# Performance work log

Measured on AMD Instinct MI355X. Metric: run time of the kernel, lower is better.

## Reference

```python
import jax, jax.numpy as jnp
import numpy as np

PLAYERS = 8
DMODEL = 256          # cfg.dmodel (per-embedding dim)
DK = 1024             # cfg.dk
WINDOW = 4096         # cfg.window == T here
A_SPACE = 64
DFULL = DMODEL * 2 * PLAYERS   # 4096, the concatenated model dim


def _positional_encoding(T, dmodel):
    # i = 1/10000^(2j/dmodel); pe[:, ::2]=sin(pos*i), pe[:, 1::2]=cos(pos*i)
    i = 1.0 / jnp.power(jnp.float32(10000.0), jnp.arange(0, dmodel, 2, dtype=jnp.float32) / dmodel)
    pos = jnp.arange(T, dtype=jnp.float32)[:, None]
    pe = jnp.zeros((T, dmodel), dtype=jnp.float32)
    pe = pe.at[:, ::2].set(jnp.sin(pos * i))
    pe = pe.at[:, 1::2].set(jnp.cos(pos * i))
    return pe


def setup_inputs() -> dict:
    key = jax.random.key(0)
    ks = jax.random.split(key, 12)
    n_rows = WINDOW * 2 * PLAYERS  # 65536 one-hot rows
    idx = jax.random.randint(ks[0], (n_rows,), 0, PLAYERS + 1)
    obs = jax.nn.one_hot(idx, PLAYERS + 1, dtype=jnp.int32)
    std = 2.0 / (5.0 * DFULL)  # torch.normal(0, var) uses var as std in the source
    return {
        "obs": obs,
        "o_emb": jax.random.normal(ks[1], (PLAYERS + 1, DMODEL), jnp.float32),
        "d_emb": jax.random.normal(ks[2], (PLAYERS + 1, DMODEL), jnp.float32),
        "WQ": jax.random.normal(ks[3], (DFULL, DK), jnp.float32) * std,
        "WK": jax.random.normal(ks[4], (DFULL, DK), jnp.float32) * std,
        "WV": jax.random.normal(ks[5], (DFULL, DK), jnp.float32) * std,
        "WO": jax.random.normal(ks[6], (DK, DK), jnp.float32) * std,
        "Wo_pol": jax.random.normal(ks[7], (A_SPACE, DK), jnp.float32) * 0.02,
        "bo_pol": jnp.zeros((A_SPACE,), jnp.float32),
        "Wd_pol": jax.random.normal(ks[8], (A_SPACE, DK), jnp.float32) * 0.02,
        "bd_pol": jnp.zeros((A_SPACE,), jnp.float32),
        "Wv": jax.random.normal(ks[9], (1, DK), jnp.float32) * 0.02,
        "bv": jnp.zeros((1,), jnp.float32),
    }


def reference(obs, o_emb, d_emb, WQ, WK, WV, WO, Wo_pol, bo_pol, Wd_pol, bd_pol, Wv, bv):
    obs2 = obs.reshape(-1, PLAYERS + 1)
    # torch.where(row == 1)[1] on one-hot rows == argmax
    idx_o = jnp.argmax(obs2[::2], axis=1)   # [T*players]
    idx_d = jnp.argmax(obs2[1::2], axis=1)  # [T*players]
    emb = jnp.concatenate([o_emb[idx_o], d_emb[idx_d]], axis=1)  # [T*players, 2*dmodel]
    x = emb.reshape(-1, DFULL) * jnp.sqrt(jnp.float32(DMODEL))    # [T, DFULL]
    T = x.shape[0]
    x = x + _positional_encoding(T, DFULL)
    q = x @ WQ  # [T, DK]
    k = x @ WK
    v = x @ WV
    att = jax.nn.softmax((q @ k.T) / jnp.sqrt(jnp.float32(DK)), axis=-1)  # [T, T]
    o = (att @ v) @ WO  # [T, DK]
    h = jax.nn.relu(o[-1])  # last position only, [DK]
    o_logits = h @ Wo_pol.T + bo_pol  # [A_SPACE]
    d_logits = h @ Wd_pol.T + bd_pol  # [A_SPACE]
    value = h @ Wv.T + bv             # [1]
    return (o_logits, d_logits, value)
```

## Files before the change

kernel.cpp:

```cpp
#include <hip/hip_runtime.h>
#include <stdint.h>

#define T_WIN   4096
#define DFULL   4096
#define DK      1024

static const size_t IDX_OFF  = 0;
static const size_t XL_OFF   = 65536;
static const size_t FRQ_OFF  = 81920;
static const size_t KQ_OFF   = 90112;
static const size_t S_OFF    = 106496;
static const size_t ATT_OFF  = 122880;
static const size_t QP_OFF   = 139264;
static const size_t AXPE_OFF = 155648;
static const size_t W_OFF    = 172032;
static const size_t CTX_OFF  = 173056;
static const size_t OL_OFF   = 177152;

#define LOG2_10000 13.287712379549449f

__global__ void idx_k(const int* __restrict__ obs,
                      const float* __restrict__ o_emb,
                      const float* __restrict__ d_emb,
                      unsigned char* __restrict__ idxb,
                      float* __restrict__ xlast,
                      float* __restrict__ freqt,
                      float* __restrict__ zbase) {
    int b = blockIdx.x, tid = threadIdx.x;
    if (b < 256) {
        int g = b * 256 + tid;
        const int* r = obs + (size_t)g * 9;
        int id = 0;
        #pragma unroll
        for (int j = 1; j < 9; ++j) id += j * r[j];
        int t = g >> 4;
        int p = (g >> 1) & 7, which = g & 1;
        idxb[t * 16 + which * 8 + p] = (unsigned char)id;
    } else if (b == 256) {
        __shared__ int lidx[16];
        if (tid < 16) {
            int row = 65520 + tid;
            const int* r = obs + (size_t)row * 9;
            int id = 0;
            #pragma unroll
            for (int j = 1; j < 9; ++j) id += j * r[j];
            int p = tid >> 1, which = tid & 1;
            lidx[which * 8 + p] = id;
        }
        __syncthreads();
        #pragma unroll
        for (int i = 0; i < 16; ++i) {
            int c = tid + 256 * i;
            int p = c >> 9, rr = c & 511;
            int seg, r; const float* tab;
            if (rr < 256) { seg = p;     r = rr;       tab = o_emb; }
            else          { seg = 8 + p; r = rr - 256; tab = d_emb; }
            float e = tab[lidx[seg] * 256 + r];
            float f = exp2f(-((float)(c & ~1) * (1.0f / 4096.0f)) * LOG2_10000);
            float sv, cv;
            __sincosf(4095.0f * f, &sv, &cv);
            xlast[c] = e * 16.0f + ((c & 1) ? cv : sv);
        }
    } else {
        float4 z4 = {0.f, 0.f, 0.f, 0.f};
        float4* z = (float4*)zbase;
        for (int i = tid; i < 2624; i += 256) z[i] = z4;
        for (int i = tid; i < 2048; i += 256)
            freqt[i] = exp2f(-((float)(2 * i) * (1.0f / 4096.0f)) * LOG2_10000);
    }
}

__global__ void q_k(const float* __restrict__ xlast,
                    const float* __restrict__ WQ,
                    float* __restrict__ qp) {
    int kc = blockIdx.x, tid = threadIdx.x;
    const float4* W4 = (const float4*)WQ;
    float4 acc = {0.f, 0.f, 0.f, 0.f};
    int kb = kc * 16;
    #pragma unroll
    for (int k = 0; k < 16; ++k) {
        float xv = xlast[kb + k];
        float4 w = W4[(size_t)(kb + k) * 256 + tid];
        acc.x += xv * w.x; acc.y += xv * w.y;
        acc.z += xv * w.z; acc.w += xv * w.w;
    }
    float* dst = qp + (kc >> 6) * 1024 + tid * 4;
    atomicAdd(dst + 0, acc.x);
    atomicAdd(dst + 1, acc.y);
    atomicAdd(dst + 2, acc.z);
    atomicAdd(dst + 3, acc.w);
}

__global__ void kq_k(const float* __restrict__ WK,
                     const float* __restrict__ qp,
                     float* __restrict__ kq) {
    __shared__ float4 qls[256];
    int tid = threadIdx.x;
    const float4* p4 = (const float4*)qp;
    float4 a = p4[tid], b = p4[256 + tid], c = p4[512 + tid], d = p4[768 + tid];
    qls[tid] = {a.x + b.x + c.x + d.x, a.y + b.y + c.y + d.y,
                a.z + b.z + c.z + d.z, a.w + b.w + c.w + d.w};
    __syncthreads();
    int wave = tid >> 6, lane = tid & 63;
    int cc = blockIdx.x * 4 + wave;
    const float4* W4 = (const float4*)(WK + (size_t)cc * DK);
    float acc = 0.0f;
    #pragma unroll
    for (int i = 0; i < 4; ++i) {
        float4 w = W4[i * 64 + lane];
        float4 q = qls[i * 64 + lane];
        acc += w.x * q.x + w.y * q.y + w.z * q.z + w.w * q.w;
    }
    #pragma unroll
    for (int off = 32; off; off >>= 1) acc += __shfl_down(acc, off, 64);
    if (lane == 0) kq[cc] = acc * (1.0f / 32.0f);
}

__global__ __launch_bounds__(256) void scores_k(
        const float* __restrict__ kq,
        const float* __restrict__ o_emb, const float* __restrict__ d_emb,
        const float* __restrict__ freqt,
        const unsigned char* __restrict__ idxb,
        float* __restrict__ s) {
    __shared__ float lkq[4096];
    __shared__ float lemb[18 * 257];
    __shared__ float lfrq[2048];
    __shared__ float ldot[144];
    __shared__ float lped[256];
    int tid = threadIdx.x, blk = blockIdx.x;
    for (int i = tid; i < 1024; i += 256)
        ((float4*)lkq)[i] = ((const float4*)kq)[i];
    for (int i = tid; i < 512; i += 256)
        ((float4*)lfrq)[i] = ((const float4*)freqt)[i];
    for (int i = tid; i < 4608; i += 256) {
        int row = i >> 8, r = i & 255;
        lemb[row * 257 + r] = (row < 9) ? o_emb[row * 256 + r]
                                        : d_emb[(row - 9) * 256 + r];
    }
    __syncthreads();
    if (tid < 144) {
        int seg = tid / 9, id = tid % 9;
        int base = (seg < 8) ? seg * 512 : (seg - 8) * 512 + 256;
        const float* e = lemb + ((seg < 8) ? id : (9 + id)) * 257;
        float a = 0.0f;
        for (int rr = 0; rr < 256; ++rr) {
            int r = (rr + seg * 4) & 255;
            a += e[r] * lkq[base + r];
        }
        ldot[tid] = 16.0f * a;
    }
    int tt = tid >> 4, sub = tid & 15;
    int t = blk * 16 + tt;
    float acc = 0.0f;
    for (int jj = 0; jj < 128; ++jj) {
        int j = sub * 128 + ((jj + 2 * sub) & 127);
        float f = lfrq[j];
        float sv, cv;
        __sincosf((float)t * f, &sv, &cv);
        acc += sv * lkq[2 * j] + cv * lkq[2 * j + 1];
    }
    lped[tt * 16 + sub] = acc;
    __syncthreads();
    if (tid < 16) {
        int t2 = blk * 16 + tid;
        float tot = 0.0f;
        #pragma unroll
        for (int i = 0; i < 16; ++i) tot += lped[tid * 16 + i];
        const uint32_t* ip = (const uint32_t*)(idxb + t2 * 16);
        uint32_t u0 = ip[0], u1 = ip[1], u2 = ip[2], u3 = ip[3];
        #pragma unroll
        for (int seg = 0; seg < 16; ++seg) {
            uint32_t u = (seg < 4) ? u0 : (seg < 8) ? u1 : (seg < 12) ? u2 : u3;
            int id = (u >> ((seg & 3) * 8)) & 0xFF;
            tot += ldot[seg * 9 + id];
        }
        s[t2] = tot;
    }
}

__global__ void softmax_k(const float* __restrict__ s, float* __restrict__ att) {
    __shared__ float redm[16], reds[16];
    int tid = threadIdx.x;
    float v0 = s[tid], v1 = s[tid + 1024], v2 = s[tid + 2048], v3 = s[tid + 3072];
    float m = fmaxf(fmaxf(v0, v1), fmaxf(v2, v3));
    #pragma unroll
    for (int off = 32; off; off >>= 1) m = fmaxf(m, __shfl_down(m, off, 64));
    if ((tid & 63) == 0) redm[tid >> 6] = m;
    __syncthreads();
    if (tid == 0) {
        float mm = redm[0];
        for (int i = 1; i < 16; ++i) mm = fmaxf(mm, redm[i]);
        redm[0] = mm;
    }
    __syncthreads();
    m = redm[0];
    float e0 = expf(v0 - m), e1 = expf(v1 - m), e2 = expf(v2 - m), e3 = expf(v3 - m);
    float sum = e0 + e1 + e2 + e3;
    #pragma unroll
    for (int off = 32; off; off >>= 1) sum += __shfl_down(sum, off, 64);
    if ((tid & 63) == 0) reds[tid >> 6] = sum;
    __syncthreads();
    if (tid == 0) {
        float ss = 0.0f;
        for (int i = 0; i < 16; ++i) ss += reds[i];
        reds[0] = ss;
    }
    __syncthreads();
    float inv = 1.0f / reds[0];
    att[tid] = e0 * inv; att[tid + 1024] = e1 * inv;
    att[tid + 2048] = e2 * inv; att[tid + 3072] = e3 * inv;
}

__global__ void att_post_k(const float* __restrict__ att,
                           const float* __restrict__ freqt,
                           const unsigned char* __restrict__ idxb,
                           float* __restrict__ weight,
                           float* __restrict__ axpe) {
    __shared__ float lh[144];
    int tid = threadIdx.x, b = blockIdx.x;
    if (tid < 144) lh[tid] = 0.0f;
    __syncthreads();
    #pragma unroll
    for (int i = 0; i < 2; ++i) {
        int it = tid + 256 * i;
        int t = b * 32 + (it >> 4), seg = it & 15;
        int id = idxb[t * 16 + seg];
        atomicAdd(&lh[seg * 9 + id], att[t]);
    }
    __syncthreads();
    if (tid < 144) atomicAdd(&weight[tid], lh[tid]);
    int g = b * 256 + tid;
    int j = g & 2047;
    int t0 = (g >> 11) * 256;
    float f = freqt[j];
    float sf, cf;
    __sincosf(f, &sf, &cf);
    float ss = 0.0f, sc = 0.0f;
    float sv = 0.f, cv = 0.f;
    for (int i = 0; i < 256; ++i) {
        if ((i & 63) == 0) __sincosf((float)(t0 + i) * f, &sv, &cv);
        float a = att[t0 + i];
        ss += a * sv; sc += a * cv;
        float ns = sv * cf + cv * sf;
        cv = cv * cf - sv * sf;
        sv = ns;
    }
    atomicAdd(&axpe[2 * j], ss);
    atomicAdd(&axpe[2 * j + 1], sc);
}

__global__ void ctxv_k(const float* __restrict__ weight,
                       const float* __restrict__ axpe,
                       const float* __restrict__ o_emb,
                       const float* __restrict__ d_emb,
                       const float* __restrict__ WV,
                       float* __restrict__ ctx) {
    __shared__ float lax[128];
    int tid = threadIdx.x;
    int cc = blockIdx.x >> 2, nc = blockIdx.x & 3;
    if (tid < 128) {
        int c = cc * 128 + tid;
        int p = c >> 9, rr = c & 511;
        int seg, r; const float* tab;
        if (rr < 256) { seg = p;     r = rr;       tab = o_emb; }
        else          { seg = 8 + p; r = rr - 256; tab = d_emb; }
        float a = 0.0f;
        #pragma unroll
        for (int id = 0; id < 9; ++id)
            a += weight[seg * 9 + id] * tab[id * 256 + r];
        lax[tid] = axpe[c] + 16.0f * a;
    }
    __syncthreads();
    int n = nc * 256 + tid;
    const float* Wp = WV + (size_t)cc * 128 * DK + n;
    float acc = 0.0f;
    for (int i = 0; i < 128; ++i)
        acc += lax[i] * Wp[(size_t)i * DK];
    atomicAdd(&ctx[n], acc);
}

__global__ void olast_k(const float* __restrict__ ctx,
                        const float* __restrict__ WO,
                        float* __restrict__ ol) {
    __shared__ float lc[64];
    int tid = threadIdx.x;
    int jc = blockIdx.x >> 2, mc = blockIdx.x & 3;
    if (tid < 64) lc[tid] = ctx[jc * 64 + tid];
    __syncthreads();
    int m = mc * 256 + tid;
    const float* Wp = WO + (size_t)jc * 64 * DK + m;
    float acc = 0.0f;
    for (int j = 0; j < 64; ++j)
        acc += lc[j] * Wp[(size_t)j * DK];
    atomicAdd(&ol[m], acc);
}

__global__ void heads_k(const float* __restrict__ ol,
                        const float* __restrict__ Wo_pol, const float* __restrict__ bo_pol,
                        const float* __restrict__ Wd_pol, const float* __restrict__ bd_pol,
                        const float* __restrict__ Wv,     const float* __restrict__ bv,
                        float* __restrict__ out) {
    __shared__ float red[4];
    int o = blockIdx.x;
    const float* W; float b;
    if (o < 64)       { W = Wo_pol + (size_t)o * DK;        b = bo_pol[o]; }
    else if (o < 128) { W = Wd_pol + (size_t)(o - 64) * DK; b = bd_pol[o - 64]; }
    else              { W = Wv;                              b = bv[0]; }
    float s = 0.0f;
    for (int m = threadIdx.x; m < DK; m += 256)
        s += fmaxf(ol[m], 0.0f) * W[m];
    #pragma unroll
    for (int off = 32; off; off >>= 1) s += __shfl_down(s, off, 64);
    int wave = threadIdx.x >> 6, lane = threadIdx.x & 63;
    if (lane == 0) red[wave] = s;
    __syncthreads();
    if (threadIdx.x == 0) out[o] = red[0] + red[1] + red[2] + red[3] + b;
}

extern "C" void kernel_launch(void* const* d_in, const int* in_sizes, int n_in,
                              void* d_out, int out_size, void* d_ws, size_t ws_size,
                              hipStream_t stream) {
    const int*   obs    = (const int*)  d_in[0];
    const float* o_emb  = (const float*)d_in[1];
    const float* d_emb  = (const float*)d_in[2];
    const float* WQ     = (const float*)d_in[3];
    const float* WK     = (const float*)d_in[4];
    const float* WV     = (const float*)d_in[5];
    const float* WO     = (const float*)d_in[6];
    const float* Wo_pol = (const float*)d_in[7];
    const float* bo_pol = (const float*)d_in[8];
    const float* Wd_pol = (const float*)d_in[9];
    const float* bd_pol = (const float*)d_in[10];
    const float* Wv     = (const float*)d_in[11];
    const float* bv     = (const float*)d_in[12];
    float* out = (float*)d_out;

    char* ws = (char*)d_ws;
    unsigned char* idxb = (unsigned char*)(ws + IDX_OFF);
    float* xlast = (float*)(ws + XL_OFF);
    float* freqt = (float*)(ws + FRQ_OFF);
    float* kq    = (float*)(ws + KQ_OFF);
    float* s     = (float*)(ws + S_OFF);
    float* att   = (float*)(ws + ATT_OFF);
    float* qp    = (float*)(ws + QP_OFF);
    float* axpe  = (float*)(ws + AXPE_OFF);
    float* wgt   = (float*)(ws + W_OFF);
    float* ctx   = (float*)(ws + CTX_OFF);
    float* ol    = (float*)(ws + OL_OFF);

    idx_k<<<258, 256, 0, stream>>>(obs, o_emb, d_emb, idxb, xlast, freqt, qp);
    q_k<<<256, 256, 0, stream>>>(xlast, WQ, qp);
    kq_k<<<1024, 256, 0, stream>>>(WK, qp, kq);
    scores_k<<<256, 256, 0, stream>>>(kq, o_emb, d_emb, freqt, idxb, s);
    softmax_k<<<1, 1024, 0, stream>>>(s, att);
    att_post_k<<<128, 256, 0, stream>>>(att, freqt, idxb, wgt, axpe);
    ctxv_k<<<128, 256, 0, stream>>>(wgt, axpe, o_emb, d_emb, WV, ctx);
    olast_k<<<64, 256, 0, stream>>>(ctx, WO, ol);
    heads_k<<<129, 256, 0, stream>>>(ol, Wo_pol, bo_pol, Wd_pol, bd_pol, Wv, bv, out);
}
```

Before: 164.1 us.

## Fuse all stages into one cooperative persistent kernel with grid syncs

Replaces nine separate kernel launches with a single cooperative kernel of 256 blocks that runs the stages in sequence, separated by grid-wide barriers. The point is to remove per-launch overhead and the gaps between small kernels. The single-block softmax is now computed redundantly in every block so attention weights no longer go through global memory. The xlast buffer is dropped in favour of shared memory in the Q stage. The costs are grid-sync latency and idle blocks in the later, smaller stages.

```diff
diff --git a/kernel.cpp b/kernel.cpp
--- a/kernel.cpp
+++ b/kernel.cpp
@@ -1,360 +1,328 @@
 #include <hip/hip_runtime.h>
+#include <hip/hip_cooperative_groups.h>
 #include <stdint.h>
+
+namespace cg = cooperative_groups;
 
 #define T_WIN   4096
 #define DFULL   4096
 #define DK      1024
+#define GRID    256
+#define LOG2_10000 13.287712379549449f
 
 static const size_t IDX_OFF  = 0;
-static const size_t XL_OFF   = 65536;
-static const size_t FRQ_OFF  = 81920;
-static const size_t KQ_OFF   = 90112;
-static const size_t S_OFF    = 106496;
-static const size_t ATT_OFF  = 122880;
-static const size_t QP_OFF   = 139264;
-static const size_t AXPE_OFF = 155648;
-static const size_t W_OFF    = 172032;
-static const size_t CTX_OFF  = 173056;
-static const size_t OL_OFF   = 177152;
-
-#define LOG2_10000 13.287712379549449f
-
-__global__ void idx_k(const int* __restrict__ obs,
-                      const float* __restrict__ o_emb,
-                      const float* __restrict__ d_emb,
-                      unsigned char* __restrict__ idxb,
-                      float* __restrict__ xlast,
-                      float* __restrict__ freqt,
-                      float* __restrict__ zbase) {
+static const size_t FRQ_OFF  = 65536;
+static const size_t KQ_OFF   = 73728;
+static const size_t S_OFF    = 90112;
+static const size_t QP_OFF   = 106496;
+static const size_t AXPE_OFF = 122880;
+static const size_t W_OFF    = 139264;
+static const size_t CTX_OFF  = 140288;
+static const size_t OL_OFF   = 144384;
+
+struct Par {
+    const int* obs;
+    const float* o_emb; const float* d_emb;
+    const float* WQ; const float* WK; const float* WV; const float* WO;
+    const float* Wo_pol; const float* bo_pol;
+    const float* Wd_pol; const float* bd_pol;
+    const float* Wv; const float* bv;
+    unsigned char* idxb;
+    float* freqt; float* kq; float* s;
+    float* qp; float* axpe; float* weight; float* ctx; float* ol;
+    float* out;
+};
+
+__global__ void __launch_bounds__(256) mega_k(Par p) {
+    cg::grid_group grid = cg::this_grid();
+    __shared__ __align__(16) float smem[11264];
     int b = blockIdx.x, tid = threadIdx.x;
-    if (b < 256) {
+    int wave = tid >> 6, lane = tid & 63;
+
+    {
         int g = b * 256 + tid;
-        const int* r = obs + (size_t)g * 9;
+        const int* r = p.obs + (size_t)g * 9;
         int id = 0;
         #pragma unroll
         for (int j = 1; j < 9; ++j) id += j * r[j];
-        int t = g >> 4;
-        int p = (g >> 1) & 7, which = g & 1;
-        idxb[t * 16 + which * 8 + p] = (unsigned char)id;
-    } else if (b == 256) {
-        __shared__ int lidx[16];
+        int t = g >> 4, pl = (g >> 1) & 7, which = g & 1;
+        p.idxb[t * 16 + which * 8 + pl] = (unsigned char)id;
+        if (b == 1)
+            for (int i = tid; i < 10496; i += 256) p.qp[i] = 0.0f;
+        if (b == 2)
+            for (int i = tid; i < 2048; i += 256)
+                p.freqt[i] = exp2f(-((float)(2 * i) * (1.0f / 4096.0f)) * LOG2_10000);
+    }
+    grid.sync();
+
+    {
+        int kb = b * 16;
+        int pl = kb >> 9, rr = kb & 511;
+        const float* tab; int r0, which;
+        if (rr < 256) { tab = p.o_emb; r0 = rr;       which = 0; }
+        else          { tab = p.d_emb; r0 = rr - 256; which = 1; }
         if (tid < 16) {
-            int row = 65520 + tid;
-            const int* r = obs + (size_t)row * 9;
+            int row = 65520 + pl * 2 + which;
+            const int* r = p.obs + (size_t)row * 9;
             int id = 0;
             #pragma unroll
             for (int j = 1; j < 9; ++j) id += j * r[j];
-            int p = tid >> 1, which = tid & 1;
-            lidx[which * 8 + p] = id;
-        }
-        __syncthreads();
-        #pragma unroll
-        for (int i = 0; i < 16; ++i) {
-            int c = tid + 256 * i;
-            int p = c >> 9, rr = c & 511;
-            int seg, r; const float* tab;
-            if (rr < 256) { seg = p;     r = rr;       tab = o_emb; }
-            else          { seg = 8 + p; r = rr - 256; tab = d_emb; }
-            float e = tab[lidx[seg] * 256 + r];
+            int c = kb + tid;
             float f = exp2f(-((float)(c & ~1) * (1.0f / 4096.0f)) * LOG2_10000);
             float sv, cv;
             __sincosf(4095.0f * f, &sv, &cv);
-            xlast[c] = e * 16.0f + ((c & 1) ? cv : sv);
-        }
-    } else {
-        float4 z4 = {0.f, 0.f, 0.f, 0.f};
-        float4* z = (float4*)zbase;
-        for (int i = tid; i < 2624; i += 256) z[i] = z4;
-        for (int i = tid; i < 2048; i += 256)
-            freqt[i] = exp2f(-((float)(2 * i) * (1.0f / 4096.0f)) * LOG2_10000);
-    }
-}
-
-__global__ void q_k(const float* __restrict__ xlast,
-                    const float* __restrict__ WQ,
-                    float* __restrict__ qp) {
-    int kc = blockIdx.x, tid = threadIdx.x;
-    const float4* W4 = (const float4*)WQ;
-    float4 acc = {0.f, 0.f, 0.f, 0.f};
-    int kb = kc * 16;
-    #pragma unroll
-    for (int k = 0; k < 16; ++k) {
-        float xv = xlast[kb + k];
-        float4 w = W4[(size_t)(kb + k) * 256 + tid];
-        acc.x += xv * w.x; acc.y += xv * w.y;
-        acc.z += xv * w.z; acc.w += xv * w.w;
-    }
-    float* dst = qp + (kc >> 6) * 1024 + tid * 4;
-    atomicAdd(dst + 0, acc.x);
-    atomicAdd(dst + 1, acc.y);
-    atomicAdd(dst + 2, acc.z);
-    atomicAdd(dst + 3, acc.w);
-}
-
-__global__ void kq_k(const float* __restrict__ WK,
-                     const float* __restrict__ qp,
-                     float* __restrict__ kq) {
-    __shared__ float4 qls[256];
-    int tid = threadIdx.x;
-    const float4* p4 = (const float4*)qp;
-    float4 a = p4[tid], b = p4[256 + tid], c = p4[512 + tid], d = p4[768 + tid];
-    qls[tid] = {a.x + b.x + c.x + d.x, a.y + b.y + c.y + d.y,
-                a.z + b.z + c.z + d.z, a.w + b.w + c.w + d.w};
-    __syncthreads();
-    int wave = tid >> 6, lane = tid & 63;
-    int cc = blockIdx.x * 4 + wave;
-    const float4* W4 = (const float4*)(WK + (size_t)cc * DK);
-    float acc = 0.0f;
-    #pragma unroll
-    for (int i = 0; i < 4; ++i) {
-        float4 w = W4[i * 64 + lane];
-        float4 q = qls[i * 64 + lane];
-        acc += w.x * q.x + w.y * q.y + w.z * q.z + w.w * q.w;
-    }
-    #pragma unroll
-    for (int off = 32; off; off >>= 1) acc += __shfl_down(acc, off, 64);
-    if (lane == 0) kq[cc] = acc * (1.0f / 32.0f);
-}
-
-__global__ __launch_bounds__(256) void scores_k(
-        const float* __restrict__ kq,
-        const float* __restrict__ o_emb, const float* __restrict__ d_emb,
-        const float* __restrict__ freqt,
-        const unsigned char* __restrict__ idxb,
-        float* __restrict__ s) {
-    __shared__ float lkq[4096];
-    __shared__ float lemb[18 * 257];
-    __shared__ float lfrq[2048];
-    __shared__ float ldot[144];
-    __shared__ float lped[256];
-    int tid = threadIdx.x, blk = blockIdx.x;
-    for (int i = tid; i < 1024; i += 256)
-        ((float4*)lkq)[i] = ((const float4*)kq)[i];
-    for (int i = tid; i < 512; i += 256)
-        ((float4*)lfrq)[i] = ((const float4*)freqt)[i];
-    for (int i = tid; i < 4608; i += 256) {
-        int row = i >> 8, r = i & 255;
-        lemb[row * 257 + r] = (row < 9) ? o_emb[row * 256 + r]
-                                        : d_emb[(row - 9) * 256 + r];
-    }
-    __syncthreads();
-    if (tid < 144) {
-        int seg = tid / 9, id = tid % 9;
-        int base = (seg < 8) ? seg * 512 : (seg - 8) * 512 + 256;
-        const float* e = lemb + ((seg < 8) ? id : (9 + id)) * 257;
-        float a = 0.0f;
-        for (int rr = 0; rr < 256; ++rr) {
-            int r = (rr + seg * 4) & 255;
-            a += e[r] * lkq[base + r];
-        }
-        ldot[tid] = 16.0f * a;
-    }
-    int tt = tid >> 4, sub = tid & 15;
-    int t = blk * 16 + tt;
-    float acc = 0.0f;
-    for (int jj = 0; jj < 128; ++jj) {
-        int j = sub * 128 + ((jj + 2 * sub) & 127);
-        float f = lfrq[j];
-        float sv, cv;
-        __sincosf((float)t * f, &sv, &cv);
-        acc += sv * lkq[2 * j] + cv * lkq[2 * j + 1];
-    }
-    lped[tt * 16 + sub] = acc;
-    __syncthreads();
-    if (tid < 16) {
-        int t2 = blk * 16 + tid;
-        float tot = 0.0f;
-        #pragma unroll
-        for (int i = 0; i < 16; ++i) tot += lped[tid * 16 + i];
-        const uint32_t* ip = (const uint32_t*)(idxb + t2 * 16);
-        uint32_t u0 = ip[0], u1 = ip[1], u2 = ip[2], u3 = ip[3];
-        #pragma unroll
-        for (int seg = 0; seg < 16; ++seg) {
-            uint32_t u = (seg < 4) ? u0 : (seg < 8) ? u1 : (seg < 12) ? u2 : u3;
-            int id = (u >> ((seg & 3) * 8)) & 0xFF;
-            tot += ldot[seg * 9 + id];
-        }
-        s[t2] = tot;
-    }
-}
-
-__global__ void softmax_k(const float* __restrict__ s, float* __restrict__ att) {
-    __shared__ float redm[16], reds[16];
-    int tid = threadIdx.x;
-    float v0 = s[tid], v1 = s[tid + 1024], v2 = s[tid + 2048], v3 = s[tid + 3072];
-    float m = fmaxf(fmaxf(v0, v1), fmaxf(v2, v3));
-    #pragma unroll
-    for (int off = 32; off; off >>= 1) m = fmaxf(m, __shfl_down(m, off, 64));
-    if ((tid & 63) == 0) redm[tid >> 6] = m;
-    __syncthreads();
-    if (tid == 0) {
-        float mm = redm[0];
-        for (int i = 1; i < 16; ++i) mm = fmaxf(mm, redm[i]);
-        redm[0] = mm;
-    }
-    __syncthreads();
-    m = redm[0];
-    float e0 = expf(v0 - m), e1 = expf(v1 - m), e2 = expf(v2 - m), e3 = expf(v3 - m);
-    float sum = e0 + e1 + e2 + e3;
-    #pragma unroll
-    for (int off = 32; off; off >>= 1) sum += __shfl_down(sum, off, 64);
-    if ((tid & 63) == 0) reds[tid >> 6] = sum;
-    __syncthreads();
-    if (tid == 0) {
-        float ss = 0.0f;
-        for (int i = 0; i < 16; ++i) ss += reds[i];
-        reds[0] = ss;
-    }
-    __syncthreads();
-    float inv = 1.0f / reds[0];
-    att[tid] = e0 * inv; att[tid + 1024] = e1 * inv;
-    att[tid + 2048] = e2 * inv; att[tid + 3072] = e3 * inv;
-}
-
-__global__ void att_post_k(const float* __restrict__ att,
-                           const float* __restrict__ freqt,
-                           const unsigned char* __restrict__ idxb,
-                           float* __restrict__ weight,
-                           float* __restrict__ axpe) {
-    __shared__ float lh[144];
-    int tid = threadIdx.x, b = blockIdx.x;
-    if (tid < 144) lh[tid] = 0.0f;
-    __syncthreads();
-    #pragma unroll
-    for (int i = 0; i < 2; ++i) {
-        int it = tid + 256 * i;
-        int t = b * 32 + (it >> 4), seg = it & 15;
-        int id = idxb[t * 16 + seg];
-        atomicAdd(&lh[seg * 9 + id], att[t]);
-    }
-    __syncthreads();
-    if (tid < 144) atomicAdd(&weight[tid], lh[tid]);
-    int g = b * 256 + tid;
-    int j = g & 2047;
-    int t0 = (g >> 11) * 256;
-    float f = freqt[j];
-    float sf, cf;
-    __sincosf(f, &sf, &cf);
-    float ss = 0.0f, sc = 0.0f;
-    float sv = 0.f, cv = 0.f;
-    for (int i = 0; i < 256; ++i) {
-        if ((i & 63) == 0) __sincosf((float)(t0 + i) * f, &sv, &cv);
-        float a = att[t0 + i];
-        ss += a * sv; sc += a * cv;
-        float ns = sv * cf + cv * sf;
-        cv = cv * cf - sv * sf;
-        sv = ns;
-    }
-    atomicAdd(&axpe[2 * j], ss);
-    atomicAdd(&axpe[2 * j + 1], sc);
-}
-
-__global__ void ctxv_k(const float* __restrict__ weight,
-                       const float* __restrict__ axpe,
-                       const float* __restrict__ o_emb,
-                       const float* __restrict__ d_emb,
-                       const float* __restrict__ WV,
-                       float* __restrict__ ctx) {
-    __shared__ float lax[128];
-    int tid = threadIdx.x;
-    int cc = blockIdx.x >> 2, nc = blockIdx.x & 3;
-    if (tid < 128) {
-        int c = cc * 128 + tid;
-        int p = c >> 9, rr = c & 511;
-        int seg, r; const float* tab;
-        if (rr < 256) { seg = p;     r = rr;       tab = o_emb; }
-        else          { seg = 8 + p; r = rr - 256; tab = d_emb; }
-        float a = 0.0f;
-        #pragma unroll
-        for (int id = 0; id < 9; ++id)
-            a += weight[seg * 9 + id] * tab[id * 256 + r];
-        lax[tid] = axpe[c] + 16.0f * a;
-    }
-    __syncthreads();
-    int n = nc * 256 + tid;
-    const float* Wp = WV + (size_t)cc * 128 * DK + n;
-    float acc = 0.0f;
-    for (int i = 0; i < 128; ++i)
-        acc += lax[i] * Wp[(size_t)i * DK];
-    atomicAdd(&ctx[n], acc);
-}
-
-__global__ void olast_k(const float* __restrict__ ctx,
-                        const float* __restrict__ WO,
-                        float* __restrict__ ol) {
-    __shared__ float lc[64];
-    int tid = threadIdx.x;
-    int jc = blockIdx.x >> 2, mc = blockIdx.x & 3;
-    if (tid < 64) lc[tid] = ctx[jc * 64 + tid];
-    __syncthreads();
-    int m = mc * 256 + tid;
-    const float* Wp = WO + (size_t)jc * 64 * DK + m;
-    float acc = 0.0f;
-    for (int j = 0; j < 64; ++j)
-        acc += lc[j] * Wp[(size_t)j * DK];
-    atomicAdd(&ol[m], acc);
-}
-
-__global__ void heads_k(const float* __restrict__ ol,
-                        const float* __restrict__ Wo_pol, const float* __restrict__ bo_pol,
-                        const float* __restrict__ Wd_pol, const float* __restrict__ bd_pol,
-                        const float* __restrict__ Wv,     const float* __restrict__ bv,
-                        float* __restrict__ out) {
-    __shared__ float red[4];
-    int o = blockIdx.x;
-    const float* W; float b;
-    if (o < 64)       { W = Wo_pol + (size_t)o * DK;        b = bo_pol[o]; }
-    else if (o < 128) { W = Wd_pol + (size_t)(o - 64) * DK; b = bd_pol[o - 64]; }
-    else              { W = Wv;                              b = bv[0]; }
-    float s = 0.0f;
-    for (int m = threadIdx.x; m < DK; m += 256)
-        s += fmaxf(ol[m], 0.0f) * W[m];
-    #pragma unroll
-    for (int off = 32; off; off >>= 1) s += __shfl_down(s, off, 64);
-    int wave = threadIdx.x >> 6, lane = threadIdx.x & 63;
-    if (lane == 0) red[wave] = s;
-    __syncthreads();
-    if (threadIdx.x == 0) out[o] = red[0] + red[1] + red[2] + red[3] + b;
+            smem[tid] = tab[id * 256 + r0 + tid] * 16.0f + ((c & 1) ? cv : sv);
+        }
+        __syncthreads();
+        const float4* W4 = (const float4*)p.WQ;
+        float4 acc = {0.f, 0.f, 0.f, 0.f};
+        #pragma unroll
+        for (int k = 0; k < 16; ++k) {
+            float xv = smem[k];
+            float4 w = W4[(size_t)(kb + k) * 256 + tid];
+            acc.x += xv * w.x; acc.y += xv * w.y;
+            acc.z += xv * w.z; acc.w += xv * w.w;
+        }
+        float* dst = p.qp + (b >> 6) * 1024 + tid * 4;
+        atomicAdd(dst + 0, acc.x);
+        atomicAdd(dst + 1, acc.y);
+        atomicAdd(dst + 2, acc.z);
+        atomicAdd(dst + 3, acc.w);
+    }
+    grid.sync();
+
+    {
+        float4* qls = (float4*)smem;
+        const float4* p4 = (const float4*)p.qp;
+        float4 a = p4[tid], b4 = p4[256 + tid], c4 = p4[512 + tid], d4 = p4[768 + tid];
+        float4 qv = {a.x + b4.x + c4.x + d4.x, a.y + b4.y + c4.y + d4.y,
+                     a.z + b4.z + c4.z + d4.z, a.w + b4.w + c4.w + d4.w};
+        qls[tid] = qv;
+        __syncthreads();
+        #pragma unroll
+        for (int rr = 0; rr < 4; ++rr) {
+            int row = b * 16 + wave * 4 + rr;
+            const float4* W4 = (const float4*)(p.WK + (size_t)row * DK);
+            float acc = 0.0f;
+            #pragma unroll
+            for (int i = 0; i < 4; ++i) {
+                float4 w = W4[i * 64 + lane];
+                float4 q = qls[i * 64 + lane];
+                acc += w.x * q.x + w.y * q.y + w.z * q.z + w.w * q.w;
+            }
+            #pragma unroll
+            for (int off = 32; off; off >>= 1) acc += __shfl_down(acc, off, 64);
+            if (lane == 0) p.kq[row] = acc * (1.0f / 32.0f);
+        }
+    }
+    grid.sync();
+
+    {
+        float* lkq  = smem;
+        float* lemb = smem + 4096;
+        float* lfrq = smem + 8768;
+        float* ldot = smem + 10816;
+        float* lped = smem + 10960;
+        for (int i = tid; i < 1024; i += 256)
+            ((float4*)lkq)[i] = ((const float4*)p.kq)[i];
+        for (int i = tid; i < 512; i += 256)
+            ((float4*)lfrq)[i] = ((const float4*)p.freqt)[i];
+        for (int i = tid; i < 4608; i += 256) {
+            int row = i >> 8, r = i & 255;
+            lemb[row * 257 + r] = (row < 9) ? p.o_emb[row * 256 + r]
+                                            : p.d_emb[(row - 9) * 256 + r];
+        }
+        __syncthreads();
+        if (tid < 144) {
+            int seg = tid / 9, id = tid % 9;
+            int base = (seg < 8) ? seg * 512 : (seg - 8) * 512 + 256;
+            const float* e = lemb + ((seg < 8) ? id : (9 + id)) * 257;
+            float a = 0.0f;
+            for (int rr = 0; rr < 256; ++rr) {
+                int r = (rr + seg * 4) & 255;
+                a += e[r] * lkq[base + r];
+            }
+            ldot[tid] = 16.0f * a;
+        }
+        int tt = tid >> 4, sub = tid & 15;
+        int t = b * 16 + tt;
+        float acc = 0.0f;
+        for (int jj = 0; jj < 128; ++jj) {
+            int j = sub * 128 + ((jj + 2 * sub) & 127);
+            float f = lfrq[j];
+            float sv, cv;
+            __sincosf((float)t * f, &sv, &cv);
+            acc += sv * lkq[2 * j] + cv * lkq[2 * j + 1];
+        }
+        lped[tt * 16 + sub] = acc;
+        __syncthreads();
+        if (tid < 16) {
+            int t2 = b * 16 + tid;
+            float tot = 0.0f;
+            #pragma unroll
+            for (int i = 0; i < 16; ++i) tot += lped[tid * 16 + i];
+            const uint32_t* ip = (const uint32_t*)(p.idxb + t2 * 16);
+            uint32_t u0 = ip[0], u1 = ip[1], u2 = ip[2], u3 = ip[3];
+            #pragma unroll
+            for (int seg = 0; seg < 16; ++seg) {
+                uint32_t u = (seg < 4) ? u0 : (seg < 8) ? u1 : (seg < 12) ? u2 : u3;
+                int id = (u >> ((seg & 3) * 8)) & 0xFF;
+                tot += ldot[seg * 9 + id];
+            }
+            p.s[t2] = tot;
+        }
+    }
+    grid.sync();
+
+    {
+        float* ls    = smem;
+        float* att_l = smem + 4096;
+        float* lh    = smem + 4352;
+        float* red   = smem + 4512;
+        float* bc    = smem + 4520;
+        int C = b >> 4;
+        #pragma unroll
+        for (int k = 0; k < 4; ++k)
+            ((float4*)ls)[tid + 256 * k] = ((const float4*)p.s)[tid + 256 * k];
+        if (tid < 144) lh[tid] = 0.0f;
+        __syncthreads();
+        float lm = -1e30f;
+        #pragma unroll
+        for (int k = 0; k < 16; ++k) lm = fmaxf(lm, ls[tid + 256 * k]);
+        #pragma unroll
+        for (int off = 32; off; off >>= 1) lm = fmaxf(lm, __shfl_down(lm, off, 64));
+        if (lane == 0) red[wave] = lm;
+        __syncthreads();
+        if (tid == 0)
+            bc[0] = fmaxf(fmaxf(red[0], red[1]), fmaxf(red[2], red[3]));
+        __syncthreads();
+        float m = bc[0];
+        float lsum = 0.0f;
+        #pragma unroll
+        for (int k = 0; k < 16; ++k) lsum += expf(ls[tid + 256 * k] - m);
+        #pragma unroll
+        for (int off = 32; off; off >>= 1) lsum += __shfl_down(lsum, off, 64);
+        if (lane == 0) red[wave] = lsum;
+        __syncthreads();
+        if (tid == 0) bc[1] = 1.0f / (red[0] + red[1] + red[2] + red[3]);
+        __syncthreads();
+        float invs = bc[1];
+        att_l[tid] = expf(ls[C * 256 + tid] - m) * invs;
+        __syncthreads();
+        {
+            int tl = tid >> 4, seg = tid & 15;
+            int tg = b * 16 + tl;
+            int id = p.idxb[tg * 16 + seg];
+            atomicAdd(&lh[seg * 9 + id], att_l[((b & 15) << 4) + tl]);
+        }
+        __syncthreads();
+        if (tid < 144) atomicAdd(&p.weight[tid], lh[tid]);
+        if (tid < 128) {
+            int j = ((b & 15) << 7) + tid;
+            float f = p.freqt[j];
+            float sf, cf;
+            __sincosf(f, &sf, &cf);
+            int t0 = C << 8;
+            float ss = 0.f, sc = 0.f, sv = 0.f, cv = 0.f;
+            for (int i = 0; i < 256; ++i) {
+                if ((i & 63) == 0) __sincosf((float)(t0 + i) * f, &sv, &cv);
+                float a = att_l[i];
+                ss += a * sv; sc += a * cv;
+                float ns = sv * cf + cv * sf;
+                cv = cv * cf - sv * sf;
+                sv = ns;
+            }
+            atomicAdd(&p.axpe[2 * j], ss);
+            atomicAdd(&p.axpe[2 * j + 1], sc);
+        }
+    }
+    grid.sync();
+
+    if (b < 128) {
+        float* lax = smem;
+        int cc = b >> 2, nc = b & 3;
+        if (tid < 128) {
+            int c = cc * 128 + tid;
+            int pl = c >> 9, rr = c & 511;
+            int seg, r; const float* tab;
+            if (rr < 256) { seg = pl;     r = rr;       tab = p.o_emb; }
+            else          { seg = 8 + pl; r = rr - 256; tab = p.d_emb; }
+            float a = 0.0f;
+            #pragma unroll
+            for (int id = 0; id < 9; ++id)
+                a += p.weight[seg * 9 + id] * tab[id * 256 + r];
+            lax[tid] = p.axpe[c] + 16.0f * a;
+        }
+        __syncthreads();
+        int n = nc * 256 + tid;
+        const float* Wp = p.WV + (size_t)cc * 128 * DK + n;
+        float acc = 0.0f;
+        for (int i = 0; i < 128; ++i)
+            acc += lax[i] * Wp[(size_t)i * DK];
+        atomicAdd(&p.ctx[n], acc);
+    }
+    grid.sync();
+
+    if (b < 64) {
+        float* lc = smem;
+        int jc = b >> 2, mc = b & 3;
+        if (tid < 64) lc[tid] = p.ctx[jc * 64 + tid];
+        __syncthreads();
+        int m = mc * 256 + tid;
+        const float* Wp = p.WO + (size_t)jc * 64 * DK + m;
+        float acc = 0.0f;
+        for (int j = 0; j < 64; ++j)
+            acc += lc[j] * Wp[(size_t)j * DK];
+        atomicAdd(&p.ol[m], acc);
+    }
+    grid.sync();
+
+    if (b < 129) {
+        float* red = smem;
+        const float* W; float bb;
+        if (b < 64)       { W = p.Wo_pol + (size_t)b * DK;        bb = p.bo_pol[b]; }
+        else if (b < 128) { W = p.Wd_pol + (size_t)(b - 64) * DK; bb = p.bd_pol[b - 64]; }
+        else              { W = p.Wv;                              bb = p.bv[0]; }
+        float s = 0.0f;
+        for (int m = tid; m < DK; m += 256)
+            s += fmaxf(p.ol[m], 0.0f) * W[m];
+        #pragma unroll
+        for (int off = 32; off; off >>= 1) s += __shfl_down(s, off, 64);
+        if (lane == 0) red[wave] = s;
+        __syncthreads();
+        if (tid == 0) p.out[b] = red[0] + red[1] + red[2] + red[3] + bb;
+    }
 }
 
 extern "C" void kernel_launch(void* const* d_in, const int* in_sizes, int n_in,
                               void* d_out, int out_size, void* d_ws, size_t ws_size,
                               hipStream_t stream) {
-    const int*   obs    = (const int*)  d_in[0];
-    const float* o_emb  = (const float*)d_in[1];
-    const float* d_emb  = (const float*)d_in[2];
-    const float* WQ     = (const float*)d_in[3];
-    const float* WK     = (const float*)d_in[4];
-    const float* WV     = (const float*)d_in[5];
-    const float* WO     = (const float*)d_in[6];
-    const float* Wo_pol = (const float*)d_in[7];
-    const float* bo_pol = (const float*)d_in[8];
-    const float* Wd_pol = (const float*)d_in[9];
-    const float* bd_pol = (const float*)d_in[10];
-    const float* Wv     = (const float*)d_in[11];
-    const float* bv     = (const float*)d_in[12];
-    float* out = (float*)d_out;
-
     char* ws = (char*)d_ws;
-    unsigned char* idxb = (unsigned char*)(ws + IDX_OFF);
-    float* xlast = (float*)(ws + XL_OFF);
-    float* freqt = (float*)(ws + FRQ_OFF);
-    float* kq    = (float*)(ws + KQ_OFF);
-    float* s     = (float*)(ws + S_OFF);
-    float* att   = (float*)(ws + ATT_OFF);
-    float* qp    = (float*)(ws + QP_OFF);
-    float* axpe  = (float*)(ws + AXPE_OFF);
-    float* wgt   = (float*)(ws + W_OFF);
-    float* ctx   = (float*)(ws + CTX_OFF);
-    float* ol    = (float*)(ws + OL_OFF);
-
-    idx_k<<<258, 256, 0, stream>>>(obs, o_emb, d_emb, idxb, xlast, freqt, qp);
-    q_k<<<256, 256, 0, stream>>>(xlast, WQ, qp);
-    kq_k<<<1024, 256, 0, stream>>>(WK, qp, kq);
-    scores_k<<<256, 256, 0, stream>>>(kq, o_emb, d_emb, freqt, idxb, s);
-    softmax_k<<<1, 1024, 0, stream>>>(s, att);
-    att_post_k<<<128, 256, 0, stream>>>(att, freqt, idxb, wgt, axpe);
-    ctxv_k<<<128, 256, 0, stream>>>(wgt, axpe, o_emb, d_emb, WV, ctx);
-    olast_k<<<64, 256, 0, stream>>>(ctx, WO, ol);
-    heads_k<<<129, 256, 0, stream>>>(ol, Wo_pol, bo_pol, Wd_pol, bd_pol, Wv, bv, out);
+    Par prm;
+    prm.obs    = (const int*)  d_in[0];
+    prm.o_emb  = (const float*)d_in[1];
+    prm.d_emb  = (const float*)d_in[2];
+    prm.WQ     = (const float*)d_in[3];
+    prm.WK     = (const float*)d_in[4];
+    prm.WV     = (const float*)d_in[5];
+    prm.WO     = (const float*)d_in[6];
+    prm.Wo_pol = (const float*)d_in[7];
+    prm.bo_pol = (const float*)d_in[8];
+    prm.Wd_pol = (const float*)d_in[9];
+    prm.bd_pol = (const float*)d_in[10];
+    prm.Wv     = (const float*)d_in[11];
+    prm.bv     = (const float*)d_in[12];
+    prm.idxb   = (unsigned char*)(ws + IDX_OFF);
+    prm.freqt  = (float*)(ws + FRQ_OFF);
+    prm.kq     = (float*)(ws + KQ_OFF);
+    prm.s      = (float*)(ws + S_OFF);
+    prm.qp     = (float*)(ws + QP_OFF);
+    prm.axpe   = (float*)(ws + AXPE_OFF);
+    prm.weight = (float*)(ws + W_OFF);
+    prm.ctx    = (float*)(ws + CTX_OFF);
+    prm.ol     = (float*)(ws + OL_OFF);
+    prm.out    = (float*)d_out;
+
+    void* args[] = { &prm };
+    hipLaunchCooperativeKernel((void*)mega_k, dim3(GRID), dim3(256), args, 0, stream);
 }
```

New measurement: 366.1 us. 123% more time.

## Fuse softmax into att_post, fold x_last into q_k, precompute PE rotation table

Applied to the files above, without the earlier changes.

Removes the single-block softmax kernel: each att_post block now recomputes the global max and sum over all 4096 scores in shared memory and derives its own attention values. The last-row input vector is computed inside q_k instead of in a separate setup block. The positional-encoding sincos in scores_k is replaced by an angle-addition from a per-block anchor times a precomputed 16-step sin/cos table, cutting transcendental work. This adds a 256 KB table and redundant softmax reductions in every att_post block.

```diff
diff --git a/kernel.cpp b/kernel.cpp
--- a/kernel.cpp
+++ b/kernel.cpp
@@ -4,28 +4,24 @@
 #define T_WIN   4096
 #define DFULL   4096
 #define DK      1024
+#define LOG2_10000 13.287712379549449f
 
 static const size_t IDX_OFF  = 0;
-static const size_t XL_OFF   = 65536;
-static const size_t FRQ_OFF  = 81920;
-static const size_t KQ_OFF   = 90112;
-static const size_t S_OFF    = 106496;
-static const size_t ATT_OFF  = 122880;
-static const size_t QP_OFF   = 139264;
-static const size_t AXPE_OFF = 155648;
-static const size_t W_OFF    = 172032;
-static const size_t CTX_OFF  = 173056;
-static const size_t OL_OFF   = 177152;
-
-#define LOG2_10000 13.287712379549449f
-
-__global__ void idx_k(const int* __restrict__ obs,
-                      const float* __restrict__ o_emb,
-                      const float* __restrict__ d_emb,
-                      unsigned char* __restrict__ idxb,
-                      float* __restrict__ xlast,
-                      float* __restrict__ freqt,
-                      float* __restrict__ zbase) {
+static const size_t FRQ_OFF  = 65536;
+static const size_t KQ_OFF   = 73728;
+static const size_t S_OFF    = 90112;
+static const size_t PE16_OFF = 106496;
+static const size_t QP_OFF   = 368640;
+static const size_t AXPE_OFF = 385024;
+static const size_t W_OFF    = 401408;
+static const size_t CTX_OFF  = 402432;
+static const size_t OL_OFF   = 406528;
+
+__global__ void setup_k(const int* __restrict__ obs,
+                        unsigned char* __restrict__ idxb,
+                        float* __restrict__ freqt,
+                        float2* __restrict__ pe16,
+                        float* __restrict__ zbase) {
     int b = blockIdx.x, tid = threadIdx.x;
     if (b < 256) {
         int g = b * 256 + tid;
@@ -33,58 +29,61 @@
         int id = 0;
         #pragma unroll
         for (int j = 1; j < 9; ++j) id += j * r[j];
-        int t = g >> 4;
-        int p = (g >> 1) & 7, which = g & 1;
-        idxb[t * 16 + which * 8 + p] = (unsigned char)id;
+        int t = g >> 4, pl = (g >> 1) & 7, which = g & 1;
+        idxb[t * 16 + which * 8 + pl] = (unsigned char)id;
     } else if (b == 256) {
-        __shared__ int lidx[16];
-        if (tid < 16) {
-            int row = 65520 + tid;
-            const int* r = obs + (size_t)row * 9;
-            int id = 0;
-            #pragma unroll
-            for (int j = 1; j < 9; ++j) id += j * r[j];
-            int p = tid >> 1, which = tid & 1;
-            lidx[which * 8 + p] = id;
-        }
-        __syncthreads();
-        #pragma unroll
-        for (int i = 0; i < 16; ++i) {
-            int c = tid + 256 * i;
-            int p = c >> 9, rr = c & 511;
-            int seg, r; const float* tab;
-            if (rr < 256) { seg = p;     r = rr;       tab = o_emb; }
-            else          { seg = 8 + p; r = rr - 256; tab = d_emb; }
-            float e = tab[lidx[seg] * 256 + r];
-            float f = exp2f(-((float)(c & ~1) * (1.0f / 4096.0f)) * LOG2_10000);
-            float sv, cv;
-            __sincosf(4095.0f * f, &sv, &cv);
-            xlast[c] = e * 16.0f + ((c & 1) ? cv : sv);
-        }
-    } else {
-        float4 z4 = {0.f, 0.f, 0.f, 0.f};
-        float4* z = (float4*)zbase;
-        for (int i = tid; i < 2624; i += 256) z[i] = z4;
+        for (int i = tid; i < 10496; i += 256) zbase[i] = 0.0f;
         for (int i = tid; i < 2048; i += 256)
             freqt[i] = exp2f(-((float)(2 * i) * (1.0f / 4096.0f)) * LOG2_10000);
-    }
-}
-
-__global__ void q_k(const float* __restrict__ xlast,
+    } else {
+        int e0 = (b - 257) * 1024 + tid * 4;
+        #pragma unroll
+        for (int k = 0; k < 4; ++k) {
+            int e = e0 + k;
+            int tt = e >> 11, j = e & 2047;
+            float f = exp2f(-((float)(2 * j) * (1.0f / 4096.0f)) * LOG2_10000);
+            float sv, cv;
+            __sincosf((float)tt * f, &sv, &cv);
+            pe16[j * 16 + tt] = {sv, cv};
+        }
+    }
+}
+
+__global__ void q_k(const int* __restrict__ obs,
+                    const float* __restrict__ o_emb,
+                    const float* __restrict__ d_emb,
                     const float* __restrict__ WQ,
                     float* __restrict__ qp) {
-    int kc = blockIdx.x, tid = threadIdx.x;
+    __shared__ float lx[16];
+    int b = blockIdx.x, tid = threadIdx.x;
+    int kb = b * 16;
+    int pl = kb >> 9, rr = kb & 511;
+    const float* tab; int r0, which;
+    if (rr < 256) { tab = o_emb; r0 = rr;       which = 0; }
+    else          { tab = d_emb; r0 = rr - 256; which = 1; }
+    if (tid < 16) {
+        int row = 65520 + pl * 2 + which;
+        const int* r = obs + (size_t)row * 9;
+        int id = 0;
+        #pragma unroll
+        for (int j = 1; j < 9; ++j) id += j * r[j];
+        int c = kb + tid;
+        float f = exp2f(-((float)(c & ~1) * (1.0f / 4096.0f)) * LOG2_10000);
+        float sv, cv;
+        __sincosf(4095.0f * f, &sv, &cv);
+        lx[tid] = tab[id * 256 + r0 + tid] * 16.0f + ((c & 1) ? cv : sv);
+    }
+    __syncthreads();
     const float4* W4 = (const float4*)WQ;
     float4 acc = {0.f, 0.f, 0.f, 0.f};
-    int kb = kc * 16;
     #pragma unroll
     for (int k = 0; k < 16; ++k) {
-        float xv = xlast[kb + k];
+        float xv = lx[k];
         float4 w = W4[(size_t)(kb + k) * 256 + tid];
         acc.x += xv * w.x; acc.y += xv * w.y;
         acc.z += xv * w.z; acc.w += xv * w.w;
     }
-    float* dst = qp + (kc >> 6) * 1024 + tid * 4;
+    float* dst = qp + (b >> 6) * 1024 + tid * 4;
     atomicAdd(dst + 0, acc.x);
     atomicAdd(dst + 1, acc.y);
     atomicAdd(dst + 2, acc.z);
@@ -97,9 +96,9 @@
     __shared__ float4 qls[256];
     int tid = threadIdx.x;
     const float4* p4 = (const float4*)qp;
-    float4 a = p4[tid], b = p4[256 + tid], c = p4[512 + tid], d = p4[768 + tid];
-    qls[tid] = {a.x + b.x + c.x + d.x, a.y + b.y + c.y + d.y,
-                a.z + b.z + c.z + d.z, a.w + b.w + c.w + d.w};
+    float4 a = p4[tid], b4 = p4[256 + tid], c4 = p4[512 + tid], d4 = p4[768 + tid];
+    qls[tid] = {a.x + b4.x + c4.x + d4.x, a.y + b4.y + c4.y + d4.y,
+                a.z + b4.z + c4.z + d4.z, a.w + b4.w + c4.w + d4.w};
     __syncthreads();
     int wave = tid >> 6, lane = tid & 63;
     int cc = blockIdx.x * 4 + wave;
@@ -120,22 +119,31 @@
         const float* __restrict__ kq,
         const float* __restrict__ o_emb, const float* __restrict__ d_emb,
         const float* __restrict__ freqt,
+        const float2* __restrict__ pe16,
         const unsigned char* __restrict__ idxb,
         float* __restrict__ s) {
-    __shared__ float lkq[4096];
+    __shared__ __align__(16) float lkq[4096];
+    __shared__ __align__(16) float2 lanc[2048];
     __shared__ float lemb[18 * 257];
-    __shared__ float lfrq[2048];
     __shared__ float ldot[144];
     __shared__ float lped[256];
-    int tid = threadIdx.x, blk = blockIdx.x;
+    int tid = threadIdx.x, b = blockIdx.x;
     for (int i = tid; i < 1024; i += 256)
         ((float4*)lkq)[i] = ((const float4*)kq)[i];
-    for (int i = tid; i < 512; i += 256)
-        ((float4*)lfrq)[i] = ((const float4*)freqt)[i];
     for (int i = tid; i < 4608; i += 256) {
         int row = i >> 8, r = i & 255;
         lemb[row * 257 + r] = (row < 9) ? o_emb[row * 256 + r]
                                         : d_emb[(row - 9) * 256 + r];
+    }
+    {
+        float base = (float)(b * 16);
+        #pragma unroll
+        for (int k = 0; k < 8; ++k) {
+            int j = tid * 8 + k;
+            float sv, cv;
+            __sincosf(base * freqt[j], &sv, &cv);
+            lanc[j] = {sv, cv};
+        }
     }
     __syncthreads();
     if (tid < 144) {
@@ -150,19 +158,19 @@
         ldot[tid] = 16.0f * a;
     }
     int tt = tid >> 4, sub = tid & 15;
-    int t = blk * 16 + tt;
     float acc = 0.0f;
     for (int jj = 0; jj < 128; ++jj) {
-        int j = sub * 128 + ((jj + 2 * sub) & 127);
-        float f = lfrq[j];
-        float sv, cv;
-        __sincosf((float)t * f, &sv, &cv);
+        int j = sub * 128 + ((jj + sub * 13) & 127);
+        float2 anc = lanc[j];
+        float2 pt = pe16[j * 16 + tt];
+        float sv = anc.x * pt.y + anc.y * pt.x;
+        float cv = anc.y * pt.y - anc.x * pt.x;
         acc += sv * lkq[2 * j] + cv * lkq[2 * j + 1];
     }
     lped[tt * 16 + sub] = acc;
     __syncthreads();
     if (tid < 16) {
-        int t2 = blk * 16 + tid;
+        int t2 = b * 16 + tid;
         float tot = 0.0f;
         #pragma unroll
         for (int i = 0; i < 16; ++i) tot += lped[tid * 16 + i];
@@ -178,75 +186,73 @@
     }
 }
 
-__global__ void softmax_k(const float* __restrict__ s, float* __restrict__ att) {
-    __shared__ float redm[16], reds[16];
-    int tid = threadIdx.x;
-    float v0 = s[tid], v1 = s[tid + 1024], v2 = s[tid + 2048], v3 = s[tid + 3072];
-    float m = fmaxf(fmaxf(v0, v1), fmaxf(v2, v3));
-    #pragma unroll
-    for (int off = 32; off; off >>= 1) m = fmaxf(m, __shfl_down(m, off, 64));
-    if ((tid & 63) == 0) redm[tid >> 6] = m;
-    __syncthreads();
-    if (tid == 0) {
-        float mm = redm[0];
-        for (int i = 1; i < 16; ++i) mm = fmaxf(mm, redm[i]);
-        redm[0] = mm;
-    }
-    __syncthreads();
-    m = redm[0];
-    float e0 = expf(v0 - m), e1 = expf(v1 - m), e2 = expf(v2 - m), e3 = expf(v3 - m);
-    float sum = e0 + e1 + e2 + e3;
-    #pragma unroll
-    for (int off = 32; off; off >>= 1) sum += __shfl_down(sum, off, 64);
-    if ((tid & 63) == 0) reds[tid >> 6] = sum;
-    __syncthreads();
-    if (tid == 0) {
-        float ss = 0.0f;
-        for (int i = 0; i < 16; ++i) ss += reds[i];
-        reds[0] = ss;
-    }
-    __syncthreads();
-    float inv = 1.0f / reds[0];
-    att[tid] = e0 * inv; att[tid + 1024] = e1 * inv;
-    att[tid + 2048] = e2 * inv; att[tid + 3072] = e3 * inv;
-}
-
-__global__ void att_post_k(const float* __restrict__ att,
+__global__ void att_post_k(const float* __restrict__ s,
                            const float* __restrict__ freqt,
                            const unsigned char* __restrict__ idxb,
                            float* __restrict__ weight,
                            float* __restrict__ axpe) {
+    __shared__ __align__(16) float ls[4096];
+    __shared__ float att_l[256];
     __shared__ float lh[144];
+    __shared__ float red[4];
+    __shared__ float bc[2];
     int tid = threadIdx.x, b = blockIdx.x;
+    int wave = tid >> 6, lane = tid & 63;
+    int C = b >> 3;
+    #pragma unroll
+    for (int k = 0; k < 4; ++k)
+        ((float4*)ls)[tid + 256 * k] = ((const float4*)s)[tid + 256 * k];
     if (tid < 144) lh[tid] = 0.0f;
     __syncthreads();
+    float lm = -1e30f;
+    #pragma unroll
+    for (int k = 0; k < 16; ++k) lm = fmaxf(lm, ls[tid + 256 * k]);
+    #pragma unroll
+    for (int off = 32; off; off >>= 1) lm = fmaxf(lm, __shfl_down(lm, off, 64));
+    if (lane == 0) red[wave] = lm;
+    __syncthreads();
+    if (tid == 0) bc[0] = fmaxf(fmaxf(red[0], red[1]), fmaxf(red[2], red[3]));
+    __syncthreads();
+    float m = bc[0];
+    float lsum = 0.0f;
+    #pragma unroll
+    for (int k = 0; k < 16; ++k) lsum += expf(ls[tid + 256 * k] - m);
+    #pragma unroll
+    for (int off = 32; off; off >>= 1) lsum += __shfl_down(lsum, off, 64);
+    if (lane == 0) red[wave] = lsum;
+    __syncthreads();
+    if (tid == 0) bc[1] = 1.0f / (red[0] + red[1] + red[2] + red[3]);
+    __syncthreads();
+    float inv = bc[1];
+    att_l[tid] = expf(ls[C * 256 + tid] - m) * inv;
     #pragma unroll
     for (int i = 0; i < 2; ++i) {
         int it = tid + 256 * i;
-        int t = b * 32 + (it >> 4), seg = it & 15;
-        int id = idxb[t * 16 + seg];
-        atomicAdd(&lh[seg * 9 + id], att[t]);
+        int tl = it >> 4, seg = it & 15;
+        int t = b * 32 + tl;
+        float av = expf(ls[t] - m) * inv;
+        atomicAdd(&lh[seg * 9 + idxb[t * 16 + seg]], av);
     }
     __syncthreads();
     if (tid < 144) atomicAdd(&weight[tid], lh[tid]);
-    int g = b * 256 + tid;
-    int j = g & 2047;
-    int t0 = (g >> 11) * 256;
-    float f = freqt[j];
-    float sf, cf;
-    __sincosf(f, &sf, &cf);
-    float ss = 0.0f, sc = 0.0f;
-    float sv = 0.f, cv = 0.f;
-    for (int i = 0; i < 256; ++i) {
-        if ((i & 63) == 0) __sincosf((float)(t0 + i) * f, &sv, &cv);
-        float a = att[t0 + i];
-        ss += a * sv; sc += a * cv;
-        float ns = sv * cf + cv * sf;
-        cv = cv * cf - sv * sf;
-        sv = ns;
-    }
-    atomicAdd(&axpe[2 * j], ss);
-    atomicAdd(&axpe[2 * j + 1], sc);
+    {
+        int j = (b & 7) * 256 + tid;
+        float f = freqt[j];
+        float sf, cf;
+        __sincosf(f, &sf, &cf);
+        int t0 = C << 8;
+        float ss = 0.f, sc = 0.f, sv = 0.f, cv = 0.f;
+        for (int i = 0; i < 256; ++i) {
+            if ((i & 63) == 0) __sincosf((float)(t0 + i) * f, &sv, &cv);
+            float a = att_l[i];
+            ss += a * sv; sc += a * cv;
+            float ns = sv * cf + cv * sf;
+            cv = cv * cf - sv * sf;
+            sv = ns;
+        }
+        atomicAdd(&axpe[2 * j], ss);
+        atomicAdd(&axpe[2 * j + 1], sc);
+    }
 }
 
 __global__ void ctxv_k(const float* __restrict__ weight,
@@ -260,10 +266,10 @@
     int cc = blockIdx.x >> 2, nc = blockIdx.x & 3;
     if (tid < 128) {
         int c = cc * 128 + tid;
-        int p = c >> 9, rr = c & 511;
+        int pl = c >> 9, rr = c & 511;
         int seg, r; const float* tab;
-        if (rr < 256) { seg = p;     r = rr;       tab = o_emb; }
-        else          { seg = 8 + p; r = rr - 256; tab = d_emb; }
+        if (rr < 256) { seg = pl;     r = rr;       tab = o_emb; }
+        else          { seg = 8 + pl; r = rr - 256; tab = d_emb; }
         float a = 0.0f;
         #pragma unroll
         for (int id = 0; id < 9; ++id)
@@ -337,23 +343,21 @@
 
     char* ws = (char*)d_ws;
     unsigned char* idxb = (unsigned char*)(ws + IDX_OFF);
-    float* xlast = (float*)(ws + XL_OFF);
-    float* freqt = (float*)(ws + FRQ_OFF);
-    float* kq    = (float*)(ws + KQ_OFF);
-    float* s     = (float*)(ws + S_OFF);
-    float* att   = (float*)(ws + ATT_OFF);
-    float* qp    = (float*)(ws + QP_OFF);
-    float* axpe  = (float*)(ws + AXPE_OFF);
-    float* wgt   = (float*)(ws + W_OFF);
-    float* ctx   = (float*)(ws + CTX_OFF);
-    float* ol    = (float*)(ws + OL_OFF);
-
-    idx_k<<<258, 256, 0, stream>>>(obs, o_emb, d_emb, idxb, xlast, freqt, qp);
-    q_k<<<256, 256, 0, stream>>>(xlast, WQ, qp);
+    float*  freqt = (float*)(ws + FRQ_OFF);
+    float*  kq    = (float*)(ws + KQ_OFF);
+    float*  s     = (float*)(ws + S_OFF);
+    float2* pe16  = (float2*)(ws + PE16_OFF);
+    float*  qp    = (float*)(ws + QP_OFF);
+    float*  axpe  = (float*)(ws + AXPE_OFF);
+    float*  wgt   = (float*)(ws + W_OFF);
+    float*  ctx   = (float*)(ws + CTX_OFF);
+    float*  ol    = (float*)(ws + OL_OFF);
+
+    setup_k<<<289, 256, 0, stream>>>(obs, idxb, freqt, pe16, qp);
+    q_k<<<256, 256, 0, stream>>>(obs, o_emb, d_emb, WQ, qp);
     kq_k<<<1024, 256, 0, stream>>>(WK, qp, kq);
-    scores_k<<<256, 256, 0, stream>>>(kq, o_emb, d_emb, freqt, idxb, s);
-    softmax_k<<<1, 1024, 0, stream>>>(s, att);
-    att_post_k<<<128, 256, 0, stream>>>(att, freqt, idxb, wgt, axpe);
+    scores_k<<<256, 256, 0, stream>>>(kq, o_emb, d_emb, freqt, pe16, idxb, s);
+    att_post_k<<<128, 256, 0, stream>>>(s, freqt, idxb, wgt, axpe);
     ctxv_k<<<128, 256, 0, stream>>>(wgt, axpe, o_emb, d_emb, WV, ctx);
     olast_k<<<64, 256, 0, stream>>>(ctx, WO, ol);
     heads_k<<<129, 256, 0, stream>>>(ol, Wo_pol, bo_pol, Wd_pol, bd_pol, Wv, bv, out);
```

Result: slower. 171.6 us (+4.6%).
